# Kernel optimization log

Hardware: AMD Instinct MI355X
Metric: run time of the kernel (lower is better)

The kernel has to match this reference:

```python
import jax, jax.numpy as jnp
import numpy as np
from jax import lax

T, P, EPS = 8, 3, 1e-5


def setup_inputs() -> dict:
    key = jax.random.key(0)
    ks = jax.random.split(key, 12)
    n, c, h, w = 16, 512, 28, 28
    r = c // 8
    sc = 1.0 / np.sqrt(c).astype(np.float32)
    return {
        "X": jax.random.normal(ks[0], (n * T, c, h, w), jnp.float32),
        "conv1_w": jax.random.normal(ks[1], (r, c, 1, 1, 1), jnp.float32) * 0.05,
        "conv1_b": jnp.zeros((r,), jnp.float32),
        "g1": jnp.ones((r,), jnp.float32),
        "b1": jnp.zeros((r,), jnp.float32),
        "m1": jax.random.normal(ks[2], (r,), jnp.float32) * 0.1,
        "v1": jax.random.uniform(ks[3], (r,), jnp.float32, 0.5, 1.5),
        "conv2_w": jax.random.normal(ks[4], (r, r, 3, 1, 1), jnp.float32) * 0.05,
        "conv2_b": jnp.zeros((r,), jnp.float32),
        "conv3_w": jax.random.normal(ks[5], (P, r, 1, 5, 5), jnp.float32) * 0.05,
        "conv3_b": jnp.zeros((P,), jnp.float32),
        "g2": jnp.ones((P,), jnp.float32),
        "b2": jnp.zeros((P,), jnp.float32),
        "m2": jax.random.normal(ks[6], (P,), jnp.float32) * 0.1,
        "v2": jax.random.uniform(ks[7], (P,), jnp.float32, 0.5, 1.5),
        "gcn0_w": jax.random.normal(ks[8], (c, c), jnp.float32) * sc,
        "gcn1_w": jax.random.normal(ks[9], (c, c), jnp.float32) * sc,
        "att_w": jax.random.normal(ks[10], (1, c), jnp.float32) * sc,
        "att_b": jnp.zeros((1,), jnp.float32),
    }


def _conv3d(x, w, b, pad):
    y = lax.conv_general_dilated(x, w, (1, 1, 1), pad,
                                 dimension_numbers=("NCDHW", "OIDHW", "NCDHW"))
    return y + b[None, :, None, None, None]


def _bn(x, g, b, m, v):
    # eval-mode BatchNorm3d folded into scale/shift
    inv = g * lax.rsqrt(v + EPS)
    return x * inv[None, :, None, None, None] + (b - m * inv)[None, :, None, None, None]


def _lrelu(x):
    return jnp.where(x >= 0, x, 0.05 * x)


def reference(X, conv1_w, conv1_b, g1, b1, m1, v1, conv2_w, conv2_b,
              conv3_w, conv3_b, g2, b2, m2, v2, gcn0_w, gcn1_w, att_w, att_b):
    nt, c, h, w = X.shape
    n = nt // T
    Xr = X.reshape(n, T, c, h, w)
    residual = Xr.mean((3, 4))                          # [n,t,c]
    Xp = jnp.transpose(Xr, (0, 2, 1, 3, 4))             # [n,c,t,h,w]

    # saliency detector
    s = _lrelu(_bn(_conv3d(Xp, conv1_w, conv1_b, [(0, 0)] * 3), g1, b1, m1, v1))
    s = _conv3d(s, conv2_w, conv2_b, [(1, 1), (0, 0), (0, 0)])
    s = _conv3d(s, conv3_w, conv3_b, [(0, 0), (2, 2), (2, 2)])
    s_map = jax.nn.sigmoid(_bn(s, g2, b2, m2, v2))      # [n,P,t,h,w]

    # weighted node pooling (avoids the [n,c,P,t,h,w] broadcast intermediate)
    nodes = jnp.einsum('ncthw,npthw->ntpc', Xp, s_map) / (h * w)
    nodes = nodes.reshape(n, T * P, c)                  # [n,N,c], N=24

    # normalized Laplacian as elementwise outer-product scaling
    A = jnp.einsum('nic,njc->nij', nodes, nodes) / c
    deg = jnp.clip(A.sum(-1), 1e-8, None)
    dinv = deg ** -0.5
    L = dinv[:, :, None] * A * dinv[:, None, :]

    # GCN (2 bias-free layers) + attention readout
    Xg = nodes
    for W in (gcn0_w, gcn1_w):
        Xg = _lrelu(L @ (Xg @ W.T))
    att = jax.nn.softmax(L @ ((Xg + nodes) @ att_w.T) + att_b, axis=1)  # [n,N,1]
    readout = (Xg * att).sum(1)                         # [n,c]
    return jnp.concatenate([readout[:, None, :], residual], axis=1)  # [n,t+1,c]
```

## Files before the change

### kernel.cpp

```cpp
#include <hip/hip_runtime.h>
#include <hip/hip_bf16.h>
#include <math.h>

#define NT 128
#define NB 16
#define TT 8
#define C 512
#define RR 64
#define HW 784
#define HH 28
#define WW 28
#define PP 3
#define NN 24
#define EPS 1e-5f

typedef __attribute__((ext_vector_type(8))) short bh8;
typedef __attribute__((ext_vector_type(4))) float f32x4;
typedef unsigned short u16;

static __device__ inline u16 f2bf(float f) {
    __hip_bfloat16 h = __float2bfloat16(f);
    return *(u16*)&h;
}
static __device__ inline float bf2f(u16 u) {
    __hip_bfloat16 h;
    *(u16*)&h = u;
    return __bfloat162float(h);
}

__global__ __launch_bounds__(256) void convA_mfma(const float* __restrict__ X,
        const float* __restrict__ W1, const float* __restrict__ cb,
        const float* __restrict__ g, const float* __restrict__ bb,
        const float* __restrict__ m, const float* __restrict__ v,
        u16* __restrict__ s1h, u16* __restrict__ s1l)
{
    __shared__ u16 Xh[32 * 72];
    __shared__ u16 Xl[32 * 72];
    __shared__ u16 Wh[4 * 64 * 8];
    __shared__ u16 Wl[4 * 64 * 8];
    __shared__ float sInv[64], sAdd[64], sCb[64];

    const int nt  = blockIdx.y;
    const int hw0 = blockIdx.x * 64;
    const int tid = threadIdx.x;

    if (tid < 64) {
        float inv = g[tid] * rsqrtf(v[tid] + EPS);
        sInv[tid] = inv;
        sAdd[tid] = bb[tid] - m[tid] * inv;
        sCb[tid]  = cb[tid];
    }

    const int sk = tid >> 3;
    const int ss = tid & 7;
    const int wr = tid >> 2;
    const int wj = tid & 3;
    const bool full = (hw0 + 64 <= HW);

    const int wv = tid >> 6;
    const int l  = tid & 63;
    const int gq = l >> 4;
    const int mm16 = l & 15;
    const int xbase = (gq * 8) * 72 + 16 * wv + (mm16 ^ ((gq & 1) << 3));

    f32x4 acc[4];
    #pragma unroll
    for (int i = 0; i < 4; ++i) acc[i] = (f32x4){0.f, 0.f, 0.f, 0.f};

    const float* Xnt = X + (size_t)nt * C * HW;

    for (int k0 = 0; k0 < C; k0 += 32) {
        {
            const float* src = Xnt + (size_t)(k0 + sk) * HW + hw0 + ss * 8;
            float x[8];
            if (full) {
                float4 a = *(const float4*)src;
                float4 b = *(const float4*)(src + 4);
                x[0] = a.x; x[1] = a.y; x[2] = a.z; x[3] = a.w;
                x[4] = b.x; x[5] = b.y; x[6] = b.z; x[7] = b.w;
            } else {
                #pragma unroll
                for (int i = 0; i < 8; ++i) {
                    int hw = hw0 + ss * 8 + i;
                    x[i] = (hw < HW) ? src[i] : 0.f;
                }
            }
            unsigned int hp[4], lp[4];
            #pragma unroll
            for (int i = 0; i < 4; ++i) {
                u16 h0 = f2bf(x[2 * i]), h1 = f2bf(x[2 * i + 1]);
                u16 l0 = f2bf(x[2 * i] - bf2f(h0));
                u16 l1 = f2bf(x[2 * i + 1] - bf2f(h1));
                hp[i] = (unsigned int)h0 | ((unsigned int)h1 << 16);
                lp[i] = (unsigned int)l0 | ((unsigned int)l1 << 16);
            }
            int xoff = sk * 72 + ((ss * 8) ^ (((sk >> 3) & 1) << 3));
            *(uint4*)&Xh[xoff] = make_uint4(hp[0], hp[1], hp[2], hp[3]);
            *(uint4*)&Xl[xoff] = make_uint4(lp[0], lp[1], lp[2], lp[3]);
        }
        {
            const float* wsrc = W1 + (size_t)wr * C + k0 + wj * 8;
            float4 a = *(const float4*)wsrc;
            float4 b = *(const float4*)(wsrc + 4);
            float x[8] = {a.x, a.y, a.z, a.w, b.x, b.y, b.z, b.w};
            unsigned int hp[4], lp[4];
            #pragma unroll
            for (int i = 0; i < 4; ++i) {
                u16 h0 = f2bf(x[2 * i]), h1 = f2bf(x[2 * i + 1]);
                u16 l0 = f2bf(x[2 * i] - bf2f(h0));
                u16 l1 = f2bf(x[2 * i + 1] - bf2f(h1));
                hp[i] = (unsigned int)h0 | ((unsigned int)h1 << 16);
                lp[i] = (unsigned int)l0 | ((unsigned int)l1 << 16);
            }
            int woff = ((wr >> 4) * 64 + (wr & 15) + 16 * wj) * 8;
            *(uint4*)&Wh[woff] = make_uint4(hp[0], hp[1], hp[2], hp[3]);
            *(uint4*)&Wl[woff] = make_uint4(lp[0], lp[1], lp[2], lp[3]);
        }
        __syncthreads();

        union { bh8 v; u16 u[8]; } fxh, fxl;
        #pragma unroll
        for (int j = 0; j < 8; ++j) {
            fxh.u[j] = Xh[xbase + j * 72];
            fxl.u[j] = Xl[xbase + j * 72];
        }
        #pragma unroll
        for (int rt = 0; rt < 4; ++rt) {
            bh8 wh = *(const bh8*)&Wh[(rt * 64 + l) * 8];
            bh8 wl = *(const bh8*)&Wl[(rt * 64 + l) * 8];
            acc[rt] = __builtin_amdgcn_mfma_f32_16x16x32_bf16(wh, fxh.v, acc[rt], 0, 0, 0);
            acc[rt] = __builtin_amdgcn_mfma_f32_16x16x32_bf16(wh, fxl.v, acc[rt], 0, 0, 0);
            acc[rt] = __builtin_amdgcn_mfma_f32_16x16x32_bf16(wl, fxh.v, acc[rt], 0, 0, 0);
        }
        __syncthreads();
    }

    const int hw = hw0 + 16 * wv + mm16;
    if (hw < HW) {
        #pragma unroll
        for (int rt = 0; rt < 4; ++rt) {
            #pragma unroll
            for (int reg = 0; reg < 4; ++reg) {
                int r = rt * 16 + 4 * gq + reg;
                float y = (acc[rt][reg] + sCb[r]) * sInv[r] + sAdd[r];
                y = (y >= 0.f) ? y : 0.05f * y;
                size_t idx = ((size_t)nt * RR + r) * HW + hw;
                u16 h = f2bf(y);
                s1h[idx] = h;
                s1l[idx] = f2bf(y - bf2f(h));
            }
        }
    }
}

__global__ __launch_bounds__(256) void convB_mfma(const u16* __restrict__ s1h,
        const u16* __restrict__ s1l, const float* __restrict__ W2,
        const float* __restrict__ cb, float* __restrict__ s2)
{
    __shared__ u16 Xh[32 * 72];
    __shared__ u16 Xl[32 * 72];
    __shared__ u16 Wh[6 * 4 * 64 * 8];
    __shared__ u16 Wl[6 * 4 * 64 * 8];

    const int nt  = blockIdx.y;
    const int n = nt >> 3, t = nt & 7;
    const int hw0 = blockIdx.x * 64;
    const int tid = threadIdx.x;
    const bool full = (hw0 + 64 <= HW);

    const int wr = tid >> 2, wj = tid & 3;
    #pragma unroll
    for (int dk = 0; dk < 6; ++dk) {
        int dt = dk >> 1, kc = dk & 1;
        const float* wsrc = W2 + (size_t)wr * 192 + (kc * 32 + wj * 8) * 3 + dt;
        float x[8];
        #pragma unroll
        for (int i = 0; i < 8; ++i) x[i] = wsrc[i * 3];
        unsigned int hp[4], lp[4];
        #pragma unroll
        for (int i = 0; i < 4; ++i) {
            u16 h0 = f2bf(x[2 * i]), h1 = f2bf(x[2 * i + 1]);
            u16 l0 = f2bf(x[2 * i] - bf2f(h0));
            u16 l1 = f2bf(x[2 * i + 1] - bf2f(h1));
            hp[i] = (unsigned int)h0 | ((unsigned int)h1 << 16);
            lp[i] = (unsigned int)l0 | ((unsigned int)l1 << 16);
        }
        int woff = dk * 2048 + ((wr >> 4) * 64 + (wr & 15) + 16 * wj) * 8;
        *(uint4*)&Wh[woff] = make_uint4(hp[0], hp[1], hp[2], hp[3]);
        *(uint4*)&Wl[woff] = make_uint4(lp[0], lp[1], lp[2], lp[3]);
    }
    __syncthreads();

    const int sk = tid >> 3, ss = tid & 7;
    const int wv = tid >> 6, l = tid & 63;
    const int gq = l >> 4, mm16 = l & 15;
    const int xbase = (gq * 8) * 72 + 16 * wv + (mm16 ^ ((gq & 1) << 3));
    const int xoff = sk * 72 + ((ss * 8) ^ (((sk >> 3) & 1) << 3));

    f32x4 acc[4];
    #pragma unroll
    for (int i = 0; i < 4; ++i) acc[i] = (f32x4){0.f, 0.f, 0.f, 0.f};

    for (int dt = 0; dt < 3; ++dt) {
        int tp = t + dt - 1;
        if (tp < 0 || tp >= TT) continue;
        const size_t pbase = (size_t)(n * TT + tp) * RR * HW;
        #pragma unroll
        for (int kc = 0; kc < 2; ++kc) {
            const size_t roff = pbase + (size_t)(kc * 32 + sk) * HW + hw0 + ss * 8;
            uint4 hv, lv;
            if (full) {
                hv = *(const uint4*)(s1h + roff);
                lv = *(const uint4*)(s1l + roff);
            } else {
                u16 ha[8], la[8];
                #pragma unroll
                for (int i = 0; i < 8; ++i) {
                    int hw = hw0 + ss * 8 + i;
                    ha[i] = (hw < HW) ? s1h[roff + i] : (u16)0;
                    la[i] = (hw < HW) ? s1l[roff + i] : (u16)0;
                }
                hv = *(uint4*)ha; lv = *(uint4*)la;
            }
            __syncthreads();
            *(uint4*)&Xh[xoff] = hv;
            *(uint4*)&Xl[xoff] = lv;
            __syncthreads();

            union { bh8 v; u16 u[8]; } fxh, fxl;
            #pragma unroll
            for (int j = 0; j < 8; ++j) {
                fxh.u[j] = Xh[xbase + j * 72];
                fxl.u[j] = Xl[xbase + j * 72];
            }
            const int dk = dt * 2 + kc;
            #pragma unroll
            for (int rt = 0; rt < 4; ++rt) {
                bh8 wh = *(const bh8*)&Wh[dk * 2048 + (rt * 64 + l) * 8];
                bh8 wl = *(const bh8*)&Wl[dk * 2048 + (rt * 64 + l) * 8];
                acc[rt] = __builtin_amdgcn_mfma_f32_16x16x32_bf16(wh, fxh.v, acc[rt], 0, 0, 0);
                acc[rt] = __builtin_amdgcn_mfma_f32_16x16x32_bf16(wh, fxl.v, acc[rt], 0, 0, 0);
                acc[rt] = __builtin_amdgcn_mfma_f32_16x16x32_bf16(wl, fxh.v, acc[rt], 0, 0, 0);
            }
        }
    }

    const int hw = hw0 + 16 * wv + mm16;
    if (hw < HW) {
        #pragma unroll
        for (int rt = 0; rt < 4; ++rt) {
            #pragma unroll
            for (int reg = 0; reg < 4; ++reg) {
                int r = rt * 16 + 4 * gq + reg;
                s2[((size_t)nt * RR + r) * HW + hw] = acc[rt][reg] + cb[r];
            }
        }
    }
}

__global__ __launch_bounds__(256) void convC_sw(const float* __restrict__ s2,
        const float* __restrict__ W3, float* __restrict__ partial)
{
    const int tid  = threadIdx.x;
    const int wave = tid >> 6;
    const int lane = tid & 63;
    const int half = lane >> 5;
    const int col  = lane & 31;
    const int item = blockIdx.x * 8 + wave * 2 + half;
    const int band = item & 3;
    const int nt   = (item >> 2) & 127;
    int cg = item >> 9;
    cg = __builtin_amdgcn_readfirstlane(cg);

    const int row0 = band * 7;
    const bool cok = (col < 28);

    float acc[3][7];
    #pragma unroll
    for (int p = 0; p < 3; ++p)
        #pragma unroll
        for (int r = 0; r < 7; ++r) acc[p][r] = 0.f;

    for (int chi = 0; chi < 8; ++chi) {
        float wgt[75];
        #pragma unroll
        for (int p = 0; p < 3; ++p)
            #pragma unroll
            for (int q = 0; q < 25; ++q)
                wgt[p * 25 + q] = W3[(size_t)(p * 64 + cg * 8 + chi) * 25 + q];

        const float* src = s2 + ((size_t)nt * RR + cg * 8 + chi) * HW;
        float w[5][5];

        #pragma unroll
        for (int rr = 0; rr < 4; ++rr) {
            int R = row0 - 2 + rr;
            bool rok = (R >= 0) & (R < HH);
            #pragma unroll
            for (int j = 0; j < 5; ++j) {
                int cc = col - 2 + j;
                bool ok = rok & cok & (cc >= 0) & (cc < WW);
                w[rr][j] = ok ? src[R * WW + cc] : 0.f;
            }
        }
        #pragma unroll
        for (int r = 0; r < 7; ++r) {
            {
                int R = row0 + 2 + r;
                bool rok = (R < HH);
                int slot = (r + 4) % 5;
                #pragma unroll
                for (int j = 0; j < 5; ++j) {
                    int cc = col - 2 + j;
                    bool ok = rok & cok & (cc >= 0) & (cc < WW);
                    w[slot][j] = ok ? src[R * WW + cc] : 0.f;
                }
            }
            #pragma unroll
            for (int p = 0; p < 3; ++p)
                #pragma unroll
                for (int dh = 0; dh < 5; ++dh)
                    #pragma unroll
                    for (int dw = 0; dw < 5; ++dw)
                        acc[p][r] += w[(r + dh) % 5][dw] * wgt[p * 25 + dh * 5 + dw];
        }
    }

    if (cok) {
        #pragma unroll
        for (int p = 0; p < 3; ++p)
            #pragma unroll
            for (int r = 0; r < 7; ++r)
                partial[(((size_t)cg * 128 + nt) * 3 + p) * HW + (row0 + r) * WW + col]
                    = acc[p][r];
    }
}

__global__ __launch_bounds__(256) void convC_fin(const float* __restrict__ partial,
        const float* __restrict__ cb, const float* __restrict__ g,
        const float* __restrict__ bb, const float* __restrict__ m,
        const float* __restrict__ v, float* __restrict__ smap)
{
    const int idx = blockIdx.x * 256 + threadIdx.x;
    const int total = 128 * 3 * HW;
    if (idx >= total) return;
    const int p = (idx / HW) % 3;
    float a = cb[p];
    #pragma unroll
    for (int gg = 0; gg < 8; ++gg) a += partial[(size_t)gg * total + idx];
    float inv = g[p] * rsqrtf(v[p] + EPS);
    float z = a * inv + (bb[p] - m[p] * inv);
    smap[idx] = 1.f / (1.f + expf(-z));
}

__global__ __launch_bounds__(256) void poolD(const float* __restrict__ X,
        const float* __restrict__ smap, float* __restrict__ nodes,
        float* __restrict__ out)
{
    const int tid = threadIdx.x;
    const int lane = tid & 63;
    const int gw = blockIdx.x * 4 + (tid >> 6);
    const int c = gw & 511;
    const int nt = gw >> 9;
    const float4* X4 = (const float4*)(X + ((size_t)nt * C + c) * HW);
    const float4* S0 = (const float4*)(smap + (size_t)nt * PP * HW);
    const float4* S1 = S0 + 196;
    const float4* S2 = S1 + 196;
    float sx = 0.f, a0 = 0.f, a1 = 0.f, a2 = 0.f;
    #pragma unroll
    for (int i = 0; i < 4; ++i) {
        int fi = i * 64 + lane;
        if (fi < 196) {
            float4 x = X4[fi];
            float4 p0 = S0[fi], p1 = S1[fi], p2 = S2[fi];
            sx += x.x + x.y + x.z + x.w;
            a0 += x.x * p0.x + x.y * p0.y + x.z * p0.z + x.w * p0.w;
            a1 += x.x * p1.x + x.y * p1.y + x.z * p1.z + x.w * p1.w;
            a2 += x.x * p2.x + x.y * p2.y + x.z * p2.z + x.w * p2.w;
        }
    }
    #pragma unroll
    for (int off = 32; off >= 1; off >>= 1) {
        sx += __shfl_xor(sx, off);
        a0 += __shfl_xor(a0, off);
        a1 += __shfl_xor(a1, off);
        a2 += __shfl_xor(a2, off);
    }
    if (lane == 0) {
        int n = nt >> 3, t = nt & 7;
        const float s = 1.f / 784.f;
        out[((size_t)n * 9 + 1 + t) * C + c] = sx * s;
        float* nd = nodes + ((size_t)n * NN + t * PP) * C + c;
        nd[0]     = a0 * s;
        nd[C]     = a1 * s;
        nd[2 * C] = a2 * s;
    }
}

__global__ __launch_bounds__(256) void graphL(const float* __restrict__ nodes,
        float* __restrict__ Lg)
{
    __shared__ float4 nds[24][129];
    __shared__ float Amat[24][24];
    __shared__ float dinv[24];
    const int n = blockIdx.x;
    const int tid = threadIdx.x;
    const float4* src = (const float4*)(nodes + (size_t)n * NN * C);
    #pragma unroll
    for (int i = 0; i < 12; ++i) {
        int fi = tid + i * 256;
        int row = fi >> 7, k4 = fi & 127;
        nds[row][k4] = src[row * 128 + k4];
    }
    __syncthreads();
    for (int pair = tid; pair < 576; pair += 256) {
        int i = pair / 24, j = pair - (pair / 24) * 24;
        const float4* ri = &nds[i][0];
        const float4* rj = &nds[j][0];
        float s = 0.f;
        for (int k = 0; k < 128; ++k) {
            float4 a = ri[k], b = rj[k];
            s += a.x * b.x + a.y * b.y + a.z * b.z + a.w * b.w;
        }
        Amat[i][j] = s * (1.f / 512.f);
    }
    __syncthreads();
    if (tid < 24) {
        float d = 0.f;
        for (int j = 0; j < 24; ++j) d += Amat[tid][j];
        d = fmaxf(d, 1e-8f);
        dinv[tid] = 1.f / sqrtf(d);
    }
    __syncthreads();
    for (int pair = tid; pair < 576; pair += 256) {
        int i = pair / 24, j = pair - (pair / 24) * 24;
        Lg[(size_t)n * 576 + pair] = dinv[i] * Amat[i][j] * dinv[j];
    }
}

__global__ __launch_bounds__(256) void gemmG(const float* __restrict__ Xin,
        const float* __restrict__ Wm, float* __restrict__ Y)
{
    __shared__ float Xs[32][36];
    __shared__ float Ws[32][66];
    const int o0 = blockIdx.x * 64;
    const int m0 = blockIdx.y * 32;
    const int tid = threadIdx.x;
    const int tr = tid >> 5;
    const int tc = tid & 31;
    float acc[4][2] = {};

    for (int k0 = 0; k0 < 512; k0 += 32) {
        {
            int ml = tid >> 3, k4 = tid & 7;
            float4 xv = *(const float4*)&Xin[(size_t)(m0 + ml) * 512 + k0 + k4 * 4];
            Xs[k4 * 4 + 0][ml] = xv.x; Xs[k4 * 4 + 1][ml] = xv.y;
            Xs[k4 * 4 + 2][ml] = xv.z; Xs[k4 * 4 + 3][ml] = xv.w;
        }
        #pragma unroll
        for (int i = 0; i < 2; ++i) {
            int idx = tid + i * 256;
            int ol = idx >> 3, k4 = idx & 7;
            float4 wv = *(const float4*)&Wm[(size_t)(o0 + ol) * 512 + k0 + k4 * 4];
            Ws[k4 * 4 + 0][ol] = wv.x; Ws[k4 * 4 + 1][ol] = wv.y;
            Ws[k4 * 4 + 2][ol] = wv.z; Ws[k4 * 4 + 3][ol] = wv.w;
        }
        __syncthreads();
        #pragma unroll
        for (int k = 0; k < 32; ++k) {
            float4 xv = *(const float4*)&Xs[k][tr * 4];
            float2 wv = *(const float2*)&Ws[k][tc * 2];
            acc[0][0] += xv.x * wv.x; acc[0][1] += xv.x * wv.y;
            acc[1][0] += xv.y * wv.x; acc[1][1] += xv.y * wv.y;
            acc[2][0] += xv.z * wv.x; acc[2][1] += xv.z * wv.y;
            acc[3][0] += xv.w * wv.x; acc[3][1] += xv.w * wv.y;
        }
        __syncthreads();
    }
    #pragma unroll
    for (int i2 = 0; i2 < 4; ++i2)
        #pragma unroll
        for (int j = 0; j < 2; ++j)
            Y[(size_t)(m0 + tr * 4 + i2) * 512 + o0 + tc * 2 + j] = acc[i2][j];
}

__global__ __launch_bounds__(256) void applyL(const float* __restrict__ G,
        const float* __restrict__ Lg, float* __restrict__ Xg)
{
    __shared__ float Ls[576];
    const int n = blockIdx.y;
    const int tid = threadIdx.x;
    for (int i = tid; i < 576; i += 256) Ls[i] = Lg[(size_t)n * 576 + i];
    __syncthreads();
    const int o = blockIdx.x * 128 + (tid & 127);
    const int ig = (tid >> 7) * 12;
    float acc[12] = {};
    const float* Gn = G + (size_t)n * NN * 512;
    for (int j = 0; j < 24; ++j) {
        float gv = Gn[j * 512 + o];
        #pragma unroll
        for (int i = 0; i < 12; ++i)
            acc[i] += Ls[(ig + i) * 24 + j] * gv;
    }
    float* Xn = Xg + (size_t)n * NN * 512;
    #pragma unroll
    for (int i = 0; i < 12; ++i) {
        float y = acc[i];
        Xn[(ig + i) * 512 + o] = (y >= 0.f) ? y : 0.05f * y;
    }
}

__global__ __launch_bounds__(256) void attE(const float* __restrict__ Xg,
        const float* __restrict__ nodes, const float* __restrict__ Lg,
        const float* __restrict__ aw, const float* __restrict__ ab,
        float* __restrict__ out)
{
    __shared__ float zs[24], ys[24], att[24], Ls[576];
    const int n = blockIdx.x;
    const int tid = threadIdx.x;
    const int lane = tid & 63, wv = tid >> 6;
    for (int i = tid; i < 576; i += 256) Ls[i] = Lg[(size_t)n * 576 + i];
    const float* Xn = Xg + (size_t)n * NN * 512;
    const float* Nn = nodes + (size_t)n * NN * 512;
    for (int i = wv; i < 24; i += 4) {
        float s = 0.f;
        #pragma unroll
        for (int kk = 0; kk < 8; ++kk) {
            int k = kk * 64 + lane;
            s += (Xn[i * 512 + k] + Nn[i * 512 + k]) * aw[k];
        }
        #pragma unroll
        for (int off = 32; off >= 1; off >>= 1) s += __shfl_xor(s, off);
        if (lane == 0) zs[i] = s;
    }
    __syncthreads();
    if (tid < 24) {
        float y = ab[0];
        for (int j = 0; j < 24; ++j) y += Ls[tid * 24 + j] * zs[j];
        ys[tid] = y;
    }
    __syncthreads();
    if (tid < 64) {
        float vv = (tid < 24) ? ys[tid] : -3.4e38f;
        float mx = vv;
        #pragma unroll
        for (int off = 32; off >= 1; off >>= 1) mx = fmaxf(mx, __shfl_xor(mx, off));
        float e = (tid < 24) ? expf(vv - mx) : 0.f;
        float ssum = e;
        #pragma unroll
        for (int off = 32; off >= 1; off >>= 1) ssum += __shfl_xor(ssum, off);
        if (tid < 24) att[tid] = e / ssum;
    }
    __syncthreads();
    for (int c2 = tid; c2 < 512; c2 += 256) {
        float r = 0.f;
        #pragma unroll
        for (int i = 0; i < 24; ++i) r += Xn[i * 512 + c2] * att[i];
        out[(size_t)n * 9 * 512 + c2] = r;
    }
}

extern "C" void kernel_launch(void* const* d_in, const int* in_sizes, int n_in,
                              void* d_out, int out_size, void* d_ws, size_t ws_size,
                              hipStream_t stream)
{
    const float* X   = (const float*)d_in[0];
    const float* w1  = (const float*)d_in[1];
    const float* b1c = (const float*)d_in[2];
    const float* g1  = (const float*)d_in[3];
    const float* b1  = (const float*)d_in[4];
    const float* m1  = (const float*)d_in[5];
    const float* v1  = (const float*)d_in[6];
    const float* w2  = (const float*)d_in[7];
    const float* b2c = (const float*)d_in[8];
    const float* w3  = (const float*)d_in[9];
    const float* b3c = (const float*)d_in[10];
    const float* g2  = (const float*)d_in[11];
    const float* b2  = (const float*)d_in[12];
    const float* m2  = (const float*)d_in[13];
    const float* v2  = (const float*)d_in[14];
    const float* gw0 = (const float*)d_in[15];
    const float* gw1 = (const float*)d_in[16];
    const float* aw  = (const float*)d_in[17];
    const float* ab  = (const float*)d_in[18];
    float* out = (float*)d_out;

    const size_t S1N = (size_t)NT * RR * HW;
    u16*   s1h   = (u16*)d_ws;
    u16*   s1l   = s1h + S1N;
    float* part  = (float*)d_ws;
    float* s2    = (float*)(s1l + S1N);
    float* smap  = s2 + S1N;
    float* nodes = smap + (size_t)NT * PP * HW;
    float* Lg    = nodes + (size_t)NB * NN * C;
    float* gt    = Lg + (size_t)NB * NN * NN;
    float* xa    = gt + (size_t)NB * NN * C;
    float* xb    = xa + (size_t)NB * NN * C;

    convA_mfma<<<dim3(13, NT), 256, 0, stream>>>(X, w1, b1c, g1, b1, m1, v1, s1h, s1l);
    convB_mfma<<<dim3(13, NT), 256, 0, stream>>>(s1h, s1l, w2, b2c, s2);
    convC_sw<<<dim3(512), 256, 0, stream>>>(s2, w3, part);
    convC_fin<<<dim3(1176), 256, 0, stream>>>(part, b3c, g2, b2, m2, v2, smap);
    poolD<<<dim3(16384), 256, 0, stream>>>(X, smap, nodes, out);
    graphL<<<dim3(NB), 256, 0, stream>>>(nodes, Lg);
    gemmG<<<dim3(8, 12), 256, 0, stream>>>(nodes, gw0, gt);
    applyL<<<dim3(4, NB), 256, 0, stream>>>(gt, Lg, xa);
    gemmG<<<dim3(8, 12), 256, 0, stream>>>(xa, gw1, gt);
    applyL<<<dim3(4, NB), 256, 0, stream>>>(gt, Lg, xb);
    attE<<<dim3(NB), 256, 0, stream>>>(xb, nodes, Lg, aw, ab, out);
}
```

Baseline: 498.3 us.

## Widen conv1/conv2 MFMA tiles to 128 pixels and pack hi/lo bf16 intermediate

convA and convB now process 128 spatial positions per block, with each wave computing a 2x4 grid of 16x16 MFMA tiles. This gives more register reuse of weight and activation fragments, and the X tile is stored in a k-contiguous, XOR-swizzled shared layout so fragments load as vectors. The hi/lo bf16 split of the intermediate s1 is packed into one u32 array, so each element needs a single load instead of two. convB stages per-dt weights inside the loop, which cuts shared memory. Global loads are now strided per k row (one element per thread across channels), which may coalesce differently, and the grid shrinks from 13 to 7 blocks per image.

After: 503.3 us. No clear change (+1.0%).

```diff
diff --git a/kernel.cpp b/kernel.cpp
--- a/kernel.cpp
+++ b/kernel.cpp
@@ -17,6 +17,7 @@
 typedef __attribute__((ext_vector_type(8))) short bh8;
 typedef __attribute__((ext_vector_type(4))) float f32x4;
 typedef unsigned short u16;
+typedef unsigned int u32;
 
 static __device__ inline u16 f2bf(float f) {
     __hip_bfloat16 h = __float2bfloat16(f);
@@ -27,21 +28,31 @@
     *(u16*)&h = u;
     return __bfloat162float(h);
 }
+static __device__ inline void pack8(const float* x, u32* hp, u32* lp) {
+    #pragma unroll
+    for (int i = 0; i < 4; ++i) {
+        u16 h0 = f2bf(x[2 * i]), h1 = f2bf(x[2 * i + 1]);
+        u16 l0 = f2bf(x[2 * i] - bf2f(h0));
+        u16 l1 = f2bf(x[2 * i + 1] - bf2f(h1));
+        hp[i] = (u32)h0 | ((u32)h1 << 16);
+        lp[i] = (u32)l0 | ((u32)l1 << 16);
+    }
+}
 
 __global__ __launch_bounds__(256) void convA_mfma(const float* __restrict__ X,
         const float* __restrict__ W1, const float* __restrict__ cb,
         const float* __restrict__ g, const float* __restrict__ bb,
         const float* __restrict__ m, const float* __restrict__ v,
-        u16* __restrict__ s1h, u16* __restrict__ s1l)
-{
-    __shared__ u16 Xh[32 * 72];
-    __shared__ u16 Xl[32 * 72];
+        u32* __restrict__ s1p)
+{
+    __shared__ u16 Xh[128 * 32];
+    __shared__ u16 Xl[128 * 32];
     __shared__ u16 Wh[4 * 64 * 8];
     __shared__ u16 Wl[4 * 64 * 8];
     __shared__ float sInv[64], sAdd[64], sCb[64];
 
     const int nt  = blockIdx.y;
-    const int hw0 = blockIdx.x * 64;
+    const int hw0 = blockIdx.x * 128;
     const int tid = threadIdx.x;
 
     if (tid < 64) {
@@ -51,208 +62,195 @@
         sCb[tid]  = cb[tid];
     }
 
-    const int sk = tid >> 3;
-    const int ss = tid & 7;
-    const int wr = tid >> 2;
-    const int wj = tid & 3;
-    const bool full = (hw0 + 64 <= HW);
-
-    const int wv = tid >> 6;
-    const int l  = tid & 63;
-    const int gq = l >> 4;
-    const int mm16 = l & 15;
-    const int xbase = (gq * 8) * 72 + 16 * wv + (mm16 ^ ((gq & 1) << 3));
-
-    f32x4 acc[4];
-    #pragma unroll
-    for (int i = 0; i < 4; ++i) acc[i] = (f32x4){0.f, 0.f, 0.f, 0.f};
+    const int hwl = tid & 127;
+    const int kg  = tid >> 7;
+    const int hw_g = hw0 + hwl;
+    const bool hok = hw_g < HW;
+    const int wr = tid >> 2, wj = tid & 3;
+    const int w  = tid >> 6, l = tid & 63;
+    const int rh = w >> 1, hh = w & 1;
+    const int gq = l >> 4, mm = l & 15;
+    const int rslot = gq ^ (mm & 3) ^ ((mm >> 2) & 3);
+
+    f32x4 acc[2][4];
+    #pragma unroll
+    for (int i = 0; i < 2; ++i)
+        #pragma unroll
+        for (int jj = 0; jj < 4; ++jj) acc[i][jj] = (f32x4){0.f, 0.f, 0.f, 0.f};
 
     const float* Xnt = X + (size_t)nt * C * HW;
 
     for (int k0 = 0; k0 < C; k0 += 32) {
+        float xv[16];
+        #pragma unroll
+        for (int j = 0; j < 16; ++j)
+            xv[j] = hok ? Xnt[(size_t)(k0 + kg * 16 + j) * HW + hw_g] : 0.f;
+        const float* wsrc = W1 + (size_t)wr * C + k0 + wj * 8;
+        float4 wa = *(const float4*)wsrc;
+        float4 wb = *(const float4*)(wsrc + 4);
+
+        __syncthreads();
+        #pragma unroll
+        for (int q = 0; q < 2; ++q) {
+            u32 hp[4], lp[4];
+            pack8(&xv[q * 8], hp, lp);
+            int slot = ((kg << 1) | q) ^ (hwl & 3) ^ ((hwl >> 2) & 3);
+            *(uint4*)&Xh[hwl * 32 + slot * 8] = make_uint4(hp[0], hp[1], hp[2], hp[3]);
+            *(uint4*)&Xl[hwl * 32 + slot * 8] = make_uint4(lp[0], lp[1], lp[2], lp[3]);
+        }
         {
-            const float* src = Xnt + (size_t)(k0 + sk) * HW + hw0 + ss * 8;
-            float x[8];
-            if (full) {
-                float4 a = *(const float4*)src;
-                float4 b = *(const float4*)(src + 4);
-                x[0] = a.x; x[1] = a.y; x[2] = a.z; x[3] = a.w;
-                x[4] = b.x; x[5] = b.y; x[6] = b.z; x[7] = b.w;
-            } else {
-                #pragma unroll
-                for (int i = 0; i < 8; ++i) {
-                    int hw = hw0 + ss * 8 + i;
-                    x[i] = (hw < HW) ? src[i] : 0.f;
-                }
-            }
-            unsigned int hp[4], lp[4];
-            #pragma unroll
-            for (int i = 0; i < 4; ++i) {
-                u16 h0 = f2bf(x[2 * i]), h1 = f2bf(x[2 * i + 1]);
-                u16 l0 = f2bf(x[2 * i] - bf2f(h0));
-                u16 l1 = f2bf(x[2 * i + 1] - bf2f(h1));
-                hp[i] = (unsigned int)h0 | ((unsigned int)h1 << 16);
-                lp[i] = (unsigned int)l0 | ((unsigned int)l1 << 16);
-            }
-            int xoff = sk * 72 + ((ss * 8) ^ (((sk >> 3) & 1) << 3));
-            *(uint4*)&Xh[xoff] = make_uint4(hp[0], hp[1], hp[2], hp[3]);
-            *(uint4*)&Xl[xoff] = make_uint4(lp[0], lp[1], lp[2], lp[3]);
-        }
-        {
-            const float* wsrc = W1 + (size_t)wr * C + k0 + wj * 8;
-            float4 a = *(const float4*)wsrc;
-            float4 b = *(const float4*)(wsrc + 4);
-            float x[8] = {a.x, a.y, a.z, a.w, b.x, b.y, b.z, b.w};
-            unsigned int hp[4], lp[4];
-            #pragma unroll
-            for (int i = 0; i < 4; ++i) {
-                u16 h0 = f2bf(x[2 * i]), h1 = f2bf(x[2 * i + 1]);
-                u16 l0 = f2bf(x[2 * i] - bf2f(h0));
-                u16 l1 = f2bf(x[2 * i + 1] - bf2f(h1));
-                hp[i] = (unsigned int)h0 | ((unsigned int)h1 << 16);
-                lp[i] = (unsigned int)l0 | ((unsigned int)l1 << 16);
-            }
+            float x[8] = {wa.x, wa.y, wa.z, wa.w, wb.x, wb.y, wb.z, wb.w};
+            u32 hp[4], lp[4];
+            pack8(x, hp, lp);
             int woff = ((wr >> 4) * 64 + (wr & 15) + 16 * wj) * 8;
             *(uint4*)&Wh[woff] = make_uint4(hp[0], hp[1], hp[2], hp[3]);
             *(uint4*)&Wl[woff] = make_uint4(lp[0], lp[1], lp[2], lp[3]);
         }
         __syncthreads();
 
-        union { bh8 v; u16 u[8]; } fxh, fxl;
-        #pragma unroll
-        for (int j = 0; j < 8; ++j) {
-            fxh.u[j] = Xh[xbase + j * 72];
-            fxl.u[j] = Xl[xbase + j * 72];
-        }
-        #pragma unroll
-        for (int rt = 0; rt < 4; ++rt) {
+        bh8 fxh[4], fxl[4];
+        #pragma unroll
+        for (int nb = 0; nb < 4; ++nb) {
+            int hwrow = (hh << 6) + (nb << 4) + mm;
+            fxh[nb] = *(const bh8*)&Xh[hwrow * 32 + rslot * 8];
+            fxl[nb] = *(const bh8*)&Xl[hwrow * 32 + rslot * 8];
+        }
+        #pragma unroll
+        for (int rr = 0; rr < 2; ++rr) {
+            int rt = (rh << 1) | rr;
             bh8 wh = *(const bh8*)&Wh[(rt * 64 + l) * 8];
             bh8 wl = *(const bh8*)&Wl[(rt * 64 + l) * 8];
-            acc[rt] = __builtin_amdgcn_mfma_f32_16x16x32_bf16(wh, fxh.v, acc[rt], 0, 0, 0);
-            acc[rt] = __builtin_amdgcn_mfma_f32_16x16x32_bf16(wh, fxl.v, acc[rt], 0, 0, 0);
-            acc[rt] = __builtin_amdgcn_mfma_f32_16x16x32_bf16(wl, fxh.v, acc[rt], 0, 0, 0);
-        }
-        __syncthreads();
-    }
-
-    const int hw = hw0 + 16 * wv + mm16;
-    if (hw < HW) {
-        #pragma unroll
-        for (int rt = 0; rt < 4; ++rt) {
-            #pragma unroll
-            for (int reg = 0; reg < 4; ++reg) {
-                int r = rt * 16 + 4 * gq + reg;
-                float y = (acc[rt][reg] + sCb[r]) * sInv[r] + sAdd[r];
-                y = (y >= 0.f) ? y : 0.05f * y;
-                size_t idx = ((size_t)nt * RR + r) * HW + hw;
-                u16 h = f2bf(y);
-                s1h[idx] = h;
-                s1l[idx] = f2bf(y - bf2f(h));
-            }
-        }
-    }
-}
-
-__global__ __launch_bounds__(256) void convB_mfma(const u16* __restrict__ s1h,
-        const u16* __restrict__ s1l, const float* __restrict__ W2,
-        const float* __restrict__ cb, float* __restrict__ s2)
-{
-    __shared__ u16 Xh[32 * 72];
-    __shared__ u16 Xl[32 * 72];
-    __shared__ u16 Wh[6 * 4 * 64 * 8];
-    __shared__ u16 Wl[6 * 4 * 64 * 8];
+            #pragma unroll
+            for (int nb = 0; nb < 4; ++nb) {
+                acc[rr][nb] = __builtin_amdgcn_mfma_f32_16x16x32_bf16(wh, fxh[nb], acc[rr][nb], 0, 0, 0);
+                acc[rr][nb] = __builtin_amdgcn_mfma_f32_16x16x32_bf16(wh, fxl[nb], acc[rr][nb], 0, 0, 0);
+                acc[rr][nb] = __builtin_amdgcn_mfma_f32_16x16x32_bf16(wl, fxh[nb], acc[rr][nb], 0, 0, 0);
+            }
+        }
+    }
+
+    #pragma unroll
+    for (int rr = 0; rr < 2; ++rr) {
+        #pragma unroll
+        for (int nb = 0; nb < 4; ++nb) {
+            int hw = hw0 + (hh << 6) + (nb << 4) + mm;
+            if (hw < HW) {
+                #pragma unroll
+                for (int reg = 0; reg < 4; ++reg) {
+                    int r = (((rh << 1) | rr) << 4) + (gq << 2) + reg;
+                    float y = (acc[rr][nb][reg] + sCb[r]) * sInv[r] + sAdd[r];
+                    y = (y >= 0.f) ? y : 0.05f * y;
+                    u16 h = f2bf(y);
+                    u16 lo = f2bf(y - bf2f(h));
+                    s1p[((size_t)nt * RR + r) * HW + hw] = (u32)h | ((u32)lo << 16);
+                }
+            }
+        }
+    }
+}
+
+__global__ __launch_bounds__(256) void convB_mfma(const u32* __restrict__ s1p,
+        const float* __restrict__ W2, const float* __restrict__ cb,
+        float* __restrict__ s2)
+{
+    __shared__ u16 Xh[128 * 32];
+    __shared__ u16 Xl[128 * 32];
+    __shared__ u16 Wh[2 * 2048];
+    __shared__ u16 Wl[2 * 2048];
 
     const int nt  = blockIdx.y;
     const int n = nt >> 3, t = nt & 7;
-    const int hw0 = blockIdx.x * 64;
+    const int hw0 = blockIdx.x * 128;
     const int tid = threadIdx.x;
-    const bool full = (hw0 + 64 <= HW);
-
+
+    const int hwl = tid & 127;
+    const int kg  = tid >> 7;
+    const int hw_g = hw0 + hwl;
+    const bool hok = hw_g < HW;
     const int wr = tid >> 2, wj = tid & 3;
-    #pragma unroll
-    for (int dk = 0; dk < 6; ++dk) {
-        int dt = dk >> 1, kc = dk & 1;
-        const float* wsrc = W2 + (size_t)wr * 192 + (kc * 32 + wj * 8) * 3 + dt;
-        float x[8];
-        #pragma unroll
-        for (int i = 0; i < 8; ++i) x[i] = wsrc[i * 3];
-        unsigned int hp[4], lp[4];
-        #pragma unroll
-        for (int i = 0; i < 4; ++i) {
-            u16 h0 = f2bf(x[2 * i]), h1 = f2bf(x[2 * i + 1]);
-            u16 l0 = f2bf(x[2 * i] - bf2f(h0));
-            u16 l1 = f2bf(x[2 * i + 1] - bf2f(h1));
-            hp[i] = (unsigned int)h0 | ((unsigned int)h1 << 16);
-            lp[i] = (unsigned int)l0 | ((unsigned int)l1 << 16);
-        }
-        int woff = dk * 2048 + ((wr >> 4) * 64 + (wr & 15) + 16 * wj) * 8;
-        *(uint4*)&Wh[woff] = make_uint4(hp[0], hp[1], hp[2], hp[3]);
-        *(uint4*)&Wl[woff] = make_uint4(lp[0], lp[1], lp[2], lp[3]);
-    }
-    __syncthreads();
-
-    const int sk = tid >> 3, ss = tid & 7;
-    const int wv = tid >> 6, l = tid & 63;
-    const int gq = l >> 4, mm16 = l & 15;
-    const int xbase = (gq * 8) * 72 + 16 * wv + (mm16 ^ ((gq & 1) << 3));
-    const int xoff = sk * 72 + ((ss * 8) ^ (((sk >> 3) & 1) << 3));
-
-    f32x4 acc[4];
-    #pragma unroll
-    for (int i = 0; i < 4; ++i) acc[i] = (f32x4){0.f, 0.f, 0.f, 0.f};
+    const int w  = tid >> 6, l = tid & 63;
+    const int rh = w >> 1, hh = w & 1;
+    const int gq = l >> 4, mm = l & 15;
+    const int rslot = gq ^ (mm & 3) ^ ((mm >> 2) & 3);
+
+    f32x4 acc[2][4];
+    #pragma unroll
+    for (int i = 0; i < 2; ++i)
+        #pragma unroll
+        for (int jj = 0; jj < 4; ++jj) acc[i][jj] = (f32x4){0.f, 0.f, 0.f, 0.f};
 
     for (int dt = 0; dt < 3; ++dt) {
         int tp = t + dt - 1;
         if (tp < 0 || tp >= TT) continue;
+        __syncthreads();
+        #pragma unroll
+        for (int kc = 0; kc < 2; ++kc) {
+            const float* wsrc = W2 + (size_t)wr * 192 + (kc * 32 + wj * 8) * 3 + dt;
+            float x[8];
+            #pragma unroll
+            for (int i = 0; i < 8; ++i) x[i] = wsrc[i * 3];
+            u32 hp[4], lp[4];
+            pack8(x, hp, lp);
+            int woff = kc * 2048 + ((wr >> 4) * 64 + (wr & 15) + 16 * wj) * 8;
+            *(uint4*)&Wh[woff] = make_uint4(hp[0], hp[1], hp[2], hp[3]);
+            *(uint4*)&Wl[woff] = make_uint4(lp[0], lp[1], lp[2], lp[3]);
+        }
         const size_t pbase = (size_t)(n * TT + tp) * RR * HW;
         #pragma unroll
         for (int kc = 0; kc < 2; ++kc) {
-            const size_t roff = pbase + (size_t)(kc * 32 + sk) * HW + hw0 + ss * 8;
-            uint4 hv, lv;
-            if (full) {
-                hv = *(const uint4*)(s1h + roff);
-                lv = *(const uint4*)(s1l + roff);
-            } else {
-                u16 ha[8], la[8];
+            u32 xv[16];
+            #pragma unroll
+            for (int j = 0; j < 16; ++j)
+                xv[j] = hok ? s1p[pbase + (size_t)(kc * 32 + kg * 16 + j) * HW + hw_g] : 0u;
+            __syncthreads();
+            #pragma unroll
+            for (int q = 0; q < 2; ++q) {
+                u32 hp[4], lp[4];
                 #pragma unroll
-                for (int i = 0; i < 8; ++i) {
-                    int hw = hw0 + ss * 8 + i;
-                    ha[i] = (hw < HW) ? s1h[roff + i] : (u16)0;
-                    la[i] = (hw < HW) ? s1l[roff + i] : (u16)0;
+                for (int i = 0; i < 4; ++i) {
+                    u32 u0 = xv[q * 8 + 2 * i], u1 = xv[q * 8 + 2 * i + 1];
+                    hp[i] = (u0 & 0xffffu) | (u1 << 16);
+                    lp[i] = (u0 >> 16) | (u1 & 0xffff0000u);
                 }
-                hv = *(uint4*)ha; lv = *(uint4*)la;
+                int slot = ((kg << 1) | q) ^ (hwl & 3) ^ ((hwl >> 2) & 3);
+                *(uint4*)&Xh[hwl * 32 + slot * 8] = make_uint4(hp[0], hp[1], hp[2], hp[3]);
+                *(uint4*)&Xl[hwl * 32 + slot * 8] = make_uint4(lp[0], lp[1], lp[2], lp[3]);
             }
             __syncthreads();
-            *(uint4*)&Xh[xoff] = hv;
-            *(uint4*)&Xl[xoff] = lv;
-            __syncthreads();
-
-            union { bh8 v; u16 u[8]; } fxh, fxl;
-            #pragma unroll
-            for (int j = 0; j < 8; ++j) {
-                fxh.u[j] = Xh[xbase + j * 72];
-                fxl.u[j] = Xl[xbase + j * 72];
-            }
-            const int dk = dt * 2 + kc;
-            #pragma unroll
-            for (int rt = 0; rt < 4; ++rt) {
-                bh8 wh = *(const bh8*)&Wh[dk * 2048 + (rt * 64 + l) * 8];
-                bh8 wl = *(const bh8*)&Wl[dk * 2048 + (rt * 64 + l) * 8];
-                acc[rt] = __builtin_amdgcn_mfma_f32_16x16x32_bf16(wh, fxh.v, acc[rt], 0, 0, 0);
-                acc[rt] = __builtin_amdgcn_mfma_f32_16x16x32_bf16(wh, fxl.v, acc[rt], 0, 0, 0);
-                acc[rt] = __builtin_amdgcn_mfma_f32_16x16x32_bf16(wl, fxh.v, acc[rt], 0, 0, 0);
-            }
-        }
-    }
-
-    const int hw = hw0 + 16 * wv + mm16;
-    if (hw < HW) {
-        #pragma unroll
-        for (int rt = 0; rt < 4; ++rt) {
-            #pragma unroll
-            for (int reg = 0; reg < 4; ++reg) {
-                int r = rt * 16 + 4 * gq + reg;
-                s2[((size_t)nt * RR + r) * HW + hw] = acc[rt][reg] + cb[r];
+
+            bh8 fxh[4], fxl[4];
+            #pragma unroll
+            for (int nb = 0; nb < 4; ++nb) {
+                int hwrow = (hh << 6) + (nb << 4) + mm;
+                fxh[nb] = *(const bh8*)&Xh[hwrow * 32 + rslot * 8];
+                fxl[nb] = *(const bh8*)&Xl[hwrow * 32 + rslot * 8];
+            }
+            #pragma unroll
+            for (int rr = 0; rr < 2; ++rr) {
+                int rt = (rh << 1) | rr;
+                bh8 wh = *(const bh8*)&Wh[kc * 2048 + (rt * 64 + l) * 8];
+                bh8 wl = *(const bh8*)&Wl[kc * 2048 + (rt * 64 + l) * 8];
+                #pragma unroll
+                for (int nb = 0; nb < 4; ++nb) {
+                    acc[rr][nb] = __builtin_amdgcn_mfma_f32_16x16x32_bf16(wh, fxh[nb], acc[rr][nb], 0, 0, 0);
+                    acc[rr][nb] = __builtin_amdgcn_mfma_f32_16x16x32_bf16(wh, fxl[nb], acc[rr][nb], 0, 0, 0);
+                    acc[rr][nb] = __builtin_amdgcn_mfma_f32_16x16x32_bf16(wl, fxh[nb], acc[rr][nb], 0, 0, 0);
+                }
+            }
+        }
+    }
+
+    #pragma unroll
+    for (int rr = 0; rr < 2; ++rr) {
+        #pragma unroll
+        for (int nb = 0; nb < 4; ++nb) {
+            int hw = hw0 + (hh << 6) + (nb << 4) + mm;
+            if (hw < HW) {
+                #pragma unroll
+                for (int reg = 0; reg < 4; ++reg) {
+                    int r = (((rh << 1) | rr) << 4) + (gq << 2) + reg;
+                    s2[((size_t)nt * RR + r) * HW + hw] = acc[rr][nb][reg] + cb[r];
+                }
             }
         }
     }
@@ -290,7 +288,7 @@
                 wgt[p * 25 + q] = W3[(size_t)(p * 64 + cg * 8 + chi) * 25 + q];
 
         const float* src = s2 + ((size_t)nt * RR + cg * 8 + chi) * HW;
-        float w[5][5];
+        float wdw[5][5];
 
         #pragma unroll
         for (int rr = 0; rr < 4; ++rr) {
@@ -300,7 +298,7 @@
             for (int j = 0; j < 5; ++j) {
                 int cc = col - 2 + j;
                 bool ok = rok & cok & (cc >= 0) & (cc < WW);
-                w[rr][j] = ok ? src[R * WW + cc] : 0.f;
+                wdw[rr][j] = ok ? src[R * WW + cc] : 0.f;
             }
         }
         #pragma unroll
@@ -313,7 +311,7 @@
                 for (int j = 0; j < 5; ++j) {
                     int cc = col - 2 + j;
                     bool ok = rok & cok & (cc >= 0) & (cc < WW);
-                    w[slot][j] = ok ? src[R * WW + cc] : 0.f;
+                    wdw[slot][j] = ok ? src[R * WW + cc] : 0.f;
                 }
             }
             #pragma unroll
@@ -322,7 +320,7 @@
                 for (int dh = 0; dh < 5; ++dh)
                     #pragma unroll
                     for (int dw = 0; dw < 5; ++dw)
-                        acc[p][r] += w[(r + dh) % 5][dw] * wgt[p * 25 + dh * 5 + dw];
+                        acc[p][r] += wdw[(r + dh) % 5][dw] * wgt[p * 25 + dh * 5 + dw];
         }
     }
 
@@ -586,10 +584,9 @@
     float* out = (float*)d_out;
 
     const size_t S1N = (size_t)NT * RR * HW;
-    u16*   s1h   = (u16*)d_ws;
-    u16*   s1l   = s1h + S1N;
+    u32*   s1p   = (u32*)d_ws;
     float* part  = (float*)d_ws;
-    float* s2    = (float*)(s1l + S1N);
+    float* s2    = (float*)(s1p + S1N);
     float* smap  = s2 + S1N;
     float* nodes = smap + (size_t)NT * PP * HW;
     float* Lg    = nodes + (size_t)NB * NN * C;
@@ -597,8 +594,8 @@
     float* xa    = gt + (size_t)NB * NN * C;
     float* xb    = xa + (size_t)NB * NN * C;
 
-    convA_mfma<<<dim3(13, NT), 256, 0, stream>>>(X, w1, b1c, g1, b1, m1, v1, s1h, s1l);
-    convB_mfma<<<dim3(13, NT), 256, 0, stream>>>(s1h, s1l, w2, b2c, s2);
+    convA_mfma<<<dim3(7, NT), 256, 0, stream>>>(X, w1, b1c, g1, b1, m1, v1, s1p);
+    convB_mfma<<<dim3(7, NT), 256, 0, stream>>>(s1p, w2, b2c, s2);
     convC_sw<<<dim3(512), 256, 0, stream>>>(s2, w3, part);
     convC_fin<<<dim3(1176), 256, 0, stream>>>(part, b3c, g2, b2, m2, v2, smap);
     poolD<<<dim3(16384), 256, 0, stream>>>(X, smap, nodes, out);
```
